# Kernel optimization log

Hardware: AMD Instinct MI355X
Metric: run time of the kernel (lower is better)

The kernel has to match this reference:

```python
import jax, jax.numpy as jnp
import numpy as np

B, S, D, E = 4, 2048, 1024, 8


def setup_inputs() -> dict:
    key = jax.random.key(0)
    ks = jax.random.split(key, 5)
    s = 0.02  # init scale
    return {
        "hidden_states": jax.random.normal(ks[0], (B, S, D), dtype=jnp.float32),
        "Wr": jax.random.normal(ks[1], (D, E), dtype=jnp.float32) * s,
        "br": jnp.zeros((E,), dtype=jnp.float32),
        "W1": jax.random.normal(ks[2], (E, D, 4 * D), dtype=jnp.float32) * s,
        "b1": jnp.zeros((E, 4 * D), dtype=jnp.float32),
        "W2": jax.random.normal(ks[3], (E, 4 * D, 2 * D), dtype=jnp.float32) * s,
        "b2": jnp.zeros((E, 2 * D), dtype=jnp.float32),
        "W3": jax.random.normal(ks[4], (E, 2 * D, D), dtype=jnp.float32) * s,
        "b3": jnp.zeros((E, D), dtype=jnp.float32),
    }


def reference(hidden_states, Wr, br, W1, b1, W2, b2, W3, b3):
    b, s, d = hidden_states.shape
    num_experts = Wr.shape[1]
    x = hidden_states.reshape(-1, d)                      # [T, D]
    # SwitchRouter: linear -> top-1 hard one-hot expert mask
    router_logits = x @ Wr + br                            # [T, E]
    expert_mask = jax.nn.one_hot(jnp.argmax(router_logits, axis=-1),
                                 num_experts, dtype=x.dtype)  # [T, E]
    out = jnp.zeros_like(x)
    # loop over small fixed expert count; dropout=0 (eval) -> identity
    for e in range(num_experts):
        h = jax.nn.gelu(x @ W1[e] + b1[e], approximate=False)   # [T, 4D]
        h = jax.nn.gelu(h @ W2[e] + b2[e], approximate=False)   # [T, 2D]
        y = h @ W3[e] + b3[e]                                   # [T, D]
        out = out + expert_mask[:, e:e + 1] * y
    return out.reshape(b, s, d)
```

## Files before the change

kernel.cpp:

```cpp
#include <hip/hip_runtime.h>


#define T_TOK 8192
#define D_DIM 1024
#define E_NUM 8

typedef __attribute__((ext_vector_type(4))) float f32x4;
typedef __attribute__((ext_vector_type(8))) short bf16x8;

__device__ __forceinline__ unsigned short f2bf(float f) {
  unsigned u = __float_as_uint(f);
  u += 0x7fffu + ((u >> 16) & 1u);
  return (unsigned short)(u >> 16);
}

__device__ __forceinline__ void gl_lds16(const void* g, void* l) {
  __builtin_amdgcn_global_load_lds(
      (const __attribute__((address_space(1))) unsigned int*)g,
      (__attribute__((address_space(3))) unsigned int*)l, 16, 0, 0);
}

__global__ void k_init(int* meta) { meta[threadIdx.x] = 0; }

__global__ __launch_bounds__(256) void k_router(
    const float* __restrict__ x, const float* __restrict__ Wr,
    const float* __restrict__ br, int* __restrict__ eid, int* __restrict__ meta) {
  int tk = blockIdx.x * 4 + (threadIdx.x >> 6);
  int l = threadIdx.x & 63;
  const float* xr = x + (size_t)tk * D_DIM;
  double acc[8];
#pragma unroll
  for (int e = 0; e < 8; ++e) acc[e] = 0.0;
  for (int it = 0; it < D_DIM / 64; ++it) {
    int d = it * 64 + l;
    double xd = (double)xr[d];
    const float4* wp = (const float4*)(Wr + (size_t)d * 8);
    float4 w0 = wp[0], w1 = wp[1];
    acc[0] += xd * (double)w0.x; acc[1] += xd * (double)w0.y;
    acc[2] += xd * (double)w0.z; acc[3] += xd * (double)w0.w;
    acc[4] += xd * (double)w1.x; acc[5] += xd * (double)w1.y;
    acc[6] += xd * (double)w1.z; acc[7] += xd * (double)w1.w;
  }
#pragma unroll
  for (int e = 0; e < 8; ++e)
    for (int off = 32; off > 0; off >>= 1)
      acc[e] += __shfl_down(acc[e], off);
  if (l == 0) {
    int best = 0; double bv = acc[0] + (double)br[0];
#pragma unroll
    for (int e = 1; e < 8; ++e) {
      double v = acc[e] + (double)br[e];
      if (v > bv) { bv = v; best = e; }
    }
    eid[tk] = best;
    atomicAdd(&meta[10 + best], 1);
  }
}

__global__ void k_prefix(int* meta) {
  if (threadIdx.x != 0) return;
  int off = 0, nt = 0;
  for (int e = 0; e < 8; ++e) {
    int c = meta[10 + e];
    meta[1 + e] = off;
    meta[20 + e] = off;
    int ntile = (c + 127) >> 7;
    for (int m = 0; m < ntile; ++m) meta[32 + nt++] = (e << 16) | m;
    off += c;
  }
  meta[9] = off;
  meta[0] = nt;
}

__global__ __launch_bounds__(256) void k_scatter(
    const float* __restrict__ x, const int* __restrict__ eid,
    int* __restrict__ meta, int* __restrict__ tokmap, unsigned short* __restrict__ Xs) {
  int tk = blockIdx.x;
  __shared__ int srow;
  if (threadIdx.x == 0) {
    int e = eid[tk];
    int i = atomicAdd(&meta[20 + e], 1);
    tokmap[i] = tk;
    srow = i;
  }
  __syncthreads();
  int i = srow;
  float4 v = ((const float4*)(x + (size_t)tk * D_DIM))[threadIdx.x];
  unsigned long long p = (unsigned long long)f2bf(v.x)
                       | ((unsigned long long)f2bf(v.y) << 16)
                       | ((unsigned long long)f2bf(v.z) << 32)
                       | ((unsigned long long)f2bf(v.w) << 48);
  *(unsigned long long*)(Xs + (size_t)i * D_DIM + threadIdx.x * 4) = p;
}

__global__ __launch_bounds__(256) void k_transpose(
    const float* __restrict__ W, unsigned short* __restrict__ Wt, int K, int N) {
  int e = blockIdx.z;
  W += (size_t)e * K * N;
  Wt += (size_t)e * K * N;
  int k0 = blockIdx.x * 32, n0 = blockIdx.y * 32;
  __shared__ float tile[32][33];
  int r = threadIdx.x >> 3, c4 = (threadIdx.x & 7) * 4;
  float4 v = *(const float4*)(W + (size_t)(k0 + r) * N + n0 + c4);
  tile[r][c4] = v.x; tile[r][c4 + 1] = v.y; tile[r][c4 + 2] = v.z; tile[r][c4 + 3] = v.w;
  __syncthreads();
  unsigned long long p = (unsigned long long)f2bf(tile[c4][r])
                       | ((unsigned long long)f2bf(tile[c4 + 1][r]) << 16)
                       | ((unsigned long long)f2bf(tile[c4 + 2][r]) << 32)
                       | ((unsigned long long)f2bf(tile[c4 + 3][r]) << 48);
  *(unsigned long long*)(Wt + (size_t)(n0 + r) * K + k0 + c4) = p;
}

template <bool GELU, bool SCATTER>
__global__ __launch_bounds__(256) void moe_gemm(
    const unsigned short* __restrict__ A, const unsigned short* __restrict__ Wt,
    const float* __restrict__ bias, const int* __restrict__ meta,
    const int* __restrict__ tokmap, unsigned short* __restrict__ Obf,
    float* __restrict__ Of, int K, int N) {
  if ((int)blockIdx.x >= meta[0]) return;
  int tl = meta[32 + blockIdx.x];
  int e = tl >> 16, mt = tl & 0xffff;
  int row0 = meta[1 + e] + mt * 128;
  int rowend = meta[2 + e];
  int ncol0 = blockIdx.y * 128;

  __shared__ char As[128 * 64 * 2];
  __shared__ char Bs[128 * 64 * 2];

  int t = threadIdx.x;
  int w = t >> 6, l = t & 63;
  int wm = w >> 1, wn = w & 1;
  size_t Kb = (size_t)K * 2;
  const char* Ab = (const char*)A;
  const char* Bb = (const char*)(Wt + (size_t)e * N * K);
  int sr = t >> 3;
  int scb = (t & 7) << 4;

  f32x4 acc[4][4];
#pragma unroll
  for (int m = 0; m < 4; ++m)
#pragma unroll
    for (int n = 0; n < 4; ++n) acc[m][n] = (f32x4)(0.0f);

  for (int kt = 0; kt < K; kt += 64) {
#pragma unroll
    for (int i = 0; i < 4; ++i) {
      int r = i * 32 + sr;
      int gr = row0 + r;
      if (gr > rowend - 1) gr = rowend - 1;
      gl_lds16(Ab + (size_t)gr * Kb + (size_t)(kt << 1) + (scb ^ ((r & 7) << 4)),
               As + (i * 32 + w * 8) * 128);
    }
#pragma unroll
    for (int i = 0; i < 4; ++i) {
      int r = i * 32 + sr;
      gl_lds16(Bb + (size_t)(ncol0 + r) * Kb + (size_t)(kt << 1) + (scb ^ ((r & 7) << 4)),
               Bs + (i * 32 + w * 8) * 128);
    }
    __syncthreads();
#pragma unroll
    for (int kh = 0; kh < 2; ++kh) {
      bf16x8 af[4], bfr[4];
      int cb = ((l >> 4) << 4) + (kh << 6);
#pragma unroll
      for (int m = 0; m < 4; ++m) {
        int row = wm * 64 + m * 16 + (l & 15);
        af[m] = *(const bf16x8*)(As + row * 128 + (cb ^ ((row & 7) << 4)));
      }
#pragma unroll
      for (int n = 0; n < 4; ++n) {
        int col = wn * 64 + n * 16 + (l & 15);
        bfr[n] = *(const bf16x8*)(Bs + col * 128 + (cb ^ ((col & 7) << 4)));
      }
#pragma unroll
      for (int m = 0; m < 4; ++m)
#pragma unroll
        for (int n = 0; n < 4; ++n)
          acc[m][n] = __builtin_amdgcn_mfma_f32_16x16x32_bf16(af[m], bfr[n], acc[m][n], 0, 0, 0);
    }
    __syncthreads();
  }

  int lr = (l >> 4) << 2, lc = l & 15;
#pragma unroll
  for (int n = 0; n < 4; ++n) {
    int col = ncol0 + wn * 64 + n * 16 + lc;
    float bv = bias[(size_t)e * N + col];
#pragma unroll
    for (int m = 0; m < 4; ++m) {
      int rb = row0 + wm * 64 + m * 16 + lr;
#pragma unroll
      for (int r = 0; r < 4; ++r) {
        int grow = rb + r;
        if (grow >= rowend) continue;
        float v = acc[m][n][r] + bv;
        if (GELU) v = 0.5f * v * (1.0f + erff(v * 0.70710678118654752f));
        if (SCATTER) Of[(size_t)tokmap[grow] * N + col] = v;
        else Obf[(size_t)grow * N + col] = f2bf(v);
      }
    }
  }
}

extern "C" void kernel_launch(void* const* d_in, const int* in_sizes, int n_in,
                              void* d_out, int out_size, void* d_ws, size_t ws_size,
                              hipStream_t stream) {
  const float* x  = (const float*)d_in[0];
  const float* Wr = (const float*)d_in[1];
  const float* br = (const float*)d_in[2];
  const float* W1 = (const float*)d_in[3];
  const float* b1 = (const float*)d_in[4];
  const float* W2 = (const float*)d_in[5];
  const float* b2 = (const float*)d_in[6];
  const float* W3 = (const float*)d_in[7];
  const float* b3 = (const float*)d_in[8];
  float* out = (float*)d_out;

  char* ws = (char*)d_ws;
  const size_t MB = 1ull << 20;
  int* meta = (int*)ws;
  int* eid = (int*)(ws + 4096);
  int* tokmap = (int*)(ws + 36864);
  unsigned short* Xs  = (unsigned short*)(ws + 1 * MB);
  unsigned short* H1  = (unsigned short*)(ws + 17 * MB);
  unsigned short* H2  = (unsigned short*)(ws + 81 * MB);
  unsigned short* W1t = (unsigned short*)(ws + 113 * MB);
  unsigned short* W2t = (unsigned short*)(ws + 177 * MB);
  unsigned short* W3t = (unsigned short*)(ws + 305 * MB);

  k_init<<<1, 256, 0, stream>>>(meta);
  k_router<<<T_TOK / 4, 256, 0, stream>>>(x, Wr, br, eid, meta);
  k_prefix<<<1, 64, 0, stream>>>(meta);
  k_scatter<<<T_TOK, 256, 0, stream>>>(x, eid, meta, tokmap, Xs);
  k_transpose<<<dim3(D_DIM / 32, 4096 / 32, E_NUM), 256, 0, stream>>>(W1, W1t, D_DIM, 4096);
  k_transpose<<<dim3(4096 / 32, 2048 / 32, E_NUM), 256, 0, stream>>>(W2, W2t, 4096, 2048);
  k_transpose<<<dim3(2048 / 32, 1024 / 32, E_NUM), 256, 0, stream>>>(W3, W3t, 2048, 1024);
  moe_gemm<true, false><<<dim3(72, 4096 / 128), 256, 0, stream>>>(
      Xs, W1t, b1, meta, tokmap, H1, nullptr, D_DIM, 4096);
  moe_gemm<true, false><<<dim3(72, 2048 / 128), 256, 0, stream>>>(
      H1, W2t, b2, meta, tokmap, H2, nullptr, 4096, 2048);
  moe_gemm<false, true><<<dim3(72, 1024 / 128), 256, 0, stream>>>(
      H2, W3t, b3, meta, tokmap, nullptr, out, 2048, 1024);
}
```

Baseline: 1.198 ms.

## Enlarge MoE GEMM tiles to 256x256 with double-buffered LDS and grid swizzle

The grouped expert GEMM moves from 128x128 tiles with 4 waves to 256x256 tiles with 8 waves. It double-buffers a 128KB LDS allocation so the next K-slice loads while MFMAs run, and uses a 1-D swizzled grid over a fixed maximum tile count. The weight transpose kernel now handles 128x128 tiles per block. The aim is better operand reuse and hidden load latency. The cost is higher register and LDS pressure (one workgroup per CU), more padding waste on partial expert tiles, and a cap of 40 row tiles that uneven routing could exceed.

Measured after the change: 1.224 ms. 2.2% more time.

```diff
diff --git a/kernel.cpp b/kernel.cpp
--- a/kernel.cpp
+++ b/kernel.cpp
@@ -4,6 +4,7 @@
 #define T_TOK 8192
 #define D_DIM 1024
 #define E_NUM 8
+#define NT_MAX 40
 
 typedef __attribute__((ext_vector_type(4))) float f32x4;
 typedef __attribute__((ext_vector_type(8))) short bf16x8;
@@ -64,7 +65,7 @@
     int c = meta[10 + e];
     meta[1 + e] = off;
     meta[20 + e] = off;
-    int ntile = (c + 127) >> 7;
+    int ntile = (c + 255) >> 8;
     for (int m = 0; m < ntile; ++m) meta[32 + nt++] = (e << 16) | m;
     off += c;
   }
@@ -95,105 +96,129 @@
 
 __global__ __launch_bounds__(256) void k_transpose(
     const float* __restrict__ W, unsigned short* __restrict__ Wt, int K, int N) {
+  __shared__ float tile[128][129];
   int e = blockIdx.z;
   W += (size_t)e * K * N;
   Wt += (size_t)e * K * N;
-  int k0 = blockIdx.x * 32, n0 = blockIdx.y * 32;
-  __shared__ float tile[32][33];
-  int r = threadIdx.x >> 3, c4 = (threadIdx.x & 7) * 4;
-  float4 v = *(const float4*)(W + (size_t)(k0 + r) * N + n0 + c4);
-  tile[r][c4] = v.x; tile[r][c4 + 1] = v.y; tile[r][c4 + 2] = v.z; tile[r][c4 + 3] = v.w;
+  int k0 = blockIdx.x * 128, n0 = blockIdx.y * 128;
+  int t = threadIdx.x;
+  int rr = t >> 5, cc = (t & 31) * 4;
+#pragma unroll
+  for (int p = 0; p < 16; ++p) {
+    int r = p * 8 + rr;
+    float4 v = *(const float4*)(W + (size_t)(k0 + r) * N + n0 + cc);
+    tile[r][cc] = v.x; tile[r][cc + 1] = v.y; tile[r][cc + 2] = v.z; tile[r][cc + 3] = v.w;
+  }
   __syncthreads();
-  unsigned long long p = (unsigned long long)f2bf(tile[c4][r])
-                       | ((unsigned long long)f2bf(tile[c4 + 1][r]) << 16)
-                       | ((unsigned long long)f2bf(tile[c4 + 2][r]) << 32)
-                       | ((unsigned long long)f2bf(tile[c4 + 3][r]) << 48);
-  *(unsigned long long*)(Wt + (size_t)(n0 + r) * K + k0 + c4) = p;
-}
-
-template <bool GELU, bool SCATTER>
-__global__ __launch_bounds__(256) void moe_gemm(
+#pragma unroll
+  for (int p = 0; p < 16; ++p) {
+    int n = p * 8 + rr;
+    unsigned long long pk = (unsigned long long)f2bf(tile[cc][n])
+      | ((unsigned long long)f2bf(tile[cc + 1][n]) << 16)
+      | ((unsigned long long)f2bf(tile[cc + 2][n]) << 32)
+      | ((unsigned long long)f2bf(tile[cc + 3][n]) << 48);
+    *(unsigned long long*)(Wt + (size_t)(n0 + n) * K + k0 + cc) = pk;
+  }
+}
+
+template <bool GELU, bool SCATTER, int NCOLS>
+__global__ __launch_bounds__(512) void moe_gemm(
     const unsigned short* __restrict__ A, const unsigned short* __restrict__ Wt,
     const float* __restrict__ bias, const int* __restrict__ meta,
     const int* __restrict__ tokmap, unsigned short* __restrict__ Obf,
-    float* __restrict__ Of, int K, int N) {
-  if ((int)blockIdx.x >= meta[0]) return;
-  int tl = meta[32 + blockIdx.x];
+    float* __restrict__ Of, int K) {
+  constexpr int N = NCOLS * 256;
+  constexpr int nwg = NT_MAX * NCOLS;
+  int swz = ((int)blockIdx.x & 7) * (nwg >> 3) + ((int)blockIdx.x >> 3);
+  int tile = swz % NT_MAX, colb = swz / NT_MAX;
+  if (tile >= meta[0]) return;
+  int tl = meta[32 + tile];
   int e = tl >> 16, mt = tl & 0xffff;
-  int row0 = meta[1 + e] + mt * 128;
+  int row0 = meta[1 + e] + mt * 256;
   int rowend = meta[2 + e];
-  int ncol0 = blockIdx.y * 128;
-
-  __shared__ char As[128 * 64 * 2];
-  __shared__ char Bs[128 * 64 * 2];
+  int ncol0 = colb * 256;
+
+  __shared__ char lds[131072];
 
   int t = threadIdx.x;
   int w = t >> 6, l = t & 63;
-  int wm = w >> 1, wn = w & 1;
+  int wm = w >> 2, wn = w & 3;
   size_t Kb = (size_t)K * 2;
   const char* Ab = (const char*)A;
   const char* Bb = (const char*)(Wt + (size_t)e * N * K);
-  int sr = t >> 3;
+  int rA = t >> 3;
   int scb = (t & 7) << 4;
 
-  f32x4 acc[4][4];
-#pragma unroll
-  for (int m = 0; m < 4; ++m)
+  f32x4 acc[8][4];
+#pragma unroll
+  for (int m = 0; m < 8; ++m)
 #pragma unroll
     for (int n = 0; n < 4; ++n) acc[m][n] = (f32x4)(0.0f);
 
-  for (int kt = 0; kt < K; kt += 64) {
+  int nk = K >> 6;
+
+  auto stage = [&](int buf, int kt) {
+    char* sA = lds + buf * 65536;
+    char* sB = sA + 32768;
+    size_t ktb = (size_t)kt << 7;
 #pragma unroll
     for (int i = 0; i < 4; ++i) {
-      int r = i * 32 + sr;
-      int gr = row0 + r;
-      if (gr > rowend - 1) gr = rowend - 1;
-      gl_lds16(Ab + (size_t)gr * Kb + (size_t)(kt << 1) + (scb ^ ((r & 7) << 4)),
-               As + (i * 32 + w * 8) * 128);
-    }
-#pragma unroll
-    for (int i = 0; i < 4; ++i) {
-      int r = i * 32 + sr;
-      gl_lds16(Bb + (size_t)(ncol0 + r) * Kb + (size_t)(kt << 1) + (scb ^ ((r & 7) << 4)),
-               Bs + (i * 32 + w * 8) * 128);
-    }
-    __syncthreads();
+      int r = i * 64 + rA;
+      int gr = row0 + r; gr = gr < rowend ? gr : rowend - 1;
+      int sw = scb ^ ((r & 7) << 4);
+      gl_lds16(Ab + (size_t)gr * Kb + ktb + sw, sA + (i * 64 + w * 8) * 128);
+      gl_lds16(Bb + (size_t)(ncol0 + r) * Kb + ktb + sw, sB + (i * 64 + w * 8) * 128);
+    }
+  };
+
+  auto compute = [&](int buf) {
+    const char* sA = lds + buf * 65536;
+    const char* sB = sA + 32768;
 #pragma unroll
     for (int kh = 0; kh < 2; ++kh) {
-      bf16x8 af[4], bfr[4];
       int cb = ((l >> 4) << 4) + (kh << 6);
-#pragma unroll
-      for (int m = 0; m < 4; ++m) {
-        int row = wm * 64 + m * 16 + (l & 15);
-        af[m] = *(const bf16x8*)(As + row * 128 + (cb ^ ((row & 7) << 4)));
+      bf16x8 af[8], bv[4];
+#pragma unroll
+      for (int m = 0; m < 8; ++m) {
+        int row = wm * 128 + m * 16 + (l & 15);
+        af[m] = *(const bf16x8*)(sA + row * 128 + (cb ^ ((row & 7) << 4)));
       }
 #pragma unroll
       for (int n = 0; n < 4; ++n) {
         int col = wn * 64 + n * 16 + (l & 15);
-        bfr[n] = *(const bf16x8*)(Bs + col * 128 + (cb ^ ((col & 7) << 4)));
+        bv[n] = *(const bf16x8*)(sB + col * 128 + (cb ^ ((col & 7) << 4)));
       }
 #pragma unroll
-      for (int m = 0; m < 4; ++m)
+      for (int m = 0; m < 8; ++m)
 #pragma unroll
         for (int n = 0; n < 4; ++n)
-          acc[m][n] = __builtin_amdgcn_mfma_f32_16x16x32_bf16(af[m], bfr[n], acc[m][n], 0, 0, 0);
-    }
+          acc[m][n] = __builtin_amdgcn_mfma_f32_16x16x32_bf16(af[m], bv[n], acc[m][n], 0, 0, 0);
+    }
+  };
+
+  stage(0, 0);
+  __syncthreads();
+  int cur = 0;
+  for (int kt = 0; kt < nk; ++kt) {
+    if (kt + 1 < nk) stage(cur ^ 1, kt + 1);
+    compute(cur);
     __syncthreads();
+    cur ^= 1;
   }
 
   int lr = (l >> 4) << 2, lc = l & 15;
 #pragma unroll
   for (int n = 0; n < 4; ++n) {
     int col = ncol0 + wn * 64 + n * 16 + lc;
-    float bv = bias[(size_t)e * N + col];
-#pragma unroll
-    for (int m = 0; m < 4; ++m) {
-      int rb = row0 + wm * 64 + m * 16 + lr;
+    float bvv = bias[(size_t)e * N + col];
+#pragma unroll
+    for (int m = 0; m < 8; ++m) {
+      int rb = row0 + wm * 128 + m * 16 + lr;
 #pragma unroll
       for (int r = 0; r < 4; ++r) {
         int grow = rb + r;
         if (grow >= rowend) continue;
-        float v = acc[m][n][r] + bv;
+        float v = acc[m][n][r] + bvv;
         if (GELU) v = 0.5f * v * (1.0f + erff(v * 0.70710678118654752f));
         if (SCATTER) Of[(size_t)tokmap[grow] * N + col] = v;
         else Obf[(size_t)grow * N + col] = f2bf(v);
@@ -232,13 +257,13 @@
   k_router<<<T_TOK / 4, 256, 0, stream>>>(x, Wr, br, eid, meta);
   k_prefix<<<1, 64, 0, stream>>>(meta);
   k_scatter<<<T_TOK, 256, 0, stream>>>(x, eid, meta, tokmap, Xs);
-  k_transpose<<<dim3(D_DIM / 32, 4096 / 32, E_NUM), 256, 0, stream>>>(W1, W1t, D_DIM, 4096);
-  k_transpose<<<dim3(4096 / 32, 2048 / 32, E_NUM), 256, 0, stream>>>(W2, W2t, 4096, 2048);
-  k_transpose<<<dim3(2048 / 32, 1024 / 32, E_NUM), 256, 0, stream>>>(W3, W3t, 2048, 1024);
-  moe_gemm<true, false><<<dim3(72, 4096 / 128), 256, 0, stream>>>(
-      Xs, W1t, b1, meta, tokmap, H1, nullptr, D_DIM, 4096);
-  moe_gemm<true, false><<<dim3(72, 2048 / 128), 256, 0, stream>>>(
-      H1, W2t, b2, meta, tokmap, H2, nullptr, 4096, 2048);
-  moe_gemm<false, true><<<dim3(72, 1024 / 128), 256, 0, stream>>>(
-      H2, W3t, b3, meta, tokmap, nullptr, out, 2048, 1024);
-}
+  k_transpose<<<dim3(D_DIM / 128, 4096 / 128, E_NUM), 256, 0, stream>>>(W1, W1t, D_DIM, 4096);
+  k_transpose<<<dim3(4096 / 128, 2048 / 128, E_NUM), 256, 0, stream>>>(W2, W2t, 4096, 2048);
+  k_transpose<<<dim3(2048 / 128, 1024 / 128, E_NUM), 256, 0, stream>>>(W3, W3t, 2048, 1024);
+  moe_gemm<true, false, 16><<<dim3(NT_MAX * 16), 512, 0, stream>>>(
+      Xs, W1t, b1, meta, tokmap, H1, nullptr, 1024);
+  moe_gemm<true, false, 8><<<dim3(NT_MAX * 8), 512, 0, stream>>>(
+      H1, W2t, b2, meta, tokmap, H2, nullptr, 4096);
+  moe_gemm<false, true, 4><<<dim3(NT_MAX * 4), 512, 0, stream>>>(
+      H2, W3t, b3, meta, tokmap, nullptr, out, 2048);
+}
```
